# Kernel tuning notes

Measured on AMD Instinct MI355X. Metric: run time of the kernel, lower is better.

## Reference

```python
import jax, jax.numpy as jnp
import numpy as np

EPS = 1e-3  # BatchNorm eps from module

def _bn(x, g, b, m, v):
    # torch BatchNorm1d (eval): (x - mean) / sqrt(var + eps) * weight + bias
    return (x - m) * (g / jnp.sqrt(v + EPS)) + b

def setup_inputs() -> dict:
    key = jax.random.key(0)
    ks = jax.random.split(key, 16)
    N, Cin, Cout, S = 1_000_000, 16, 64, 20_000
    inputs = jax.random.normal(ks[0], (N, Cin), dtype=jnp.float32)
    unq_inv = jax.random.randint(ks[1], (N,), 0, S, dtype=jnp.int32)

    def bn_params(k, c):
        k1, k2, k3, k4 = jax.random.split(k, 4)
        return (1.0 + 0.01 * jax.random.normal(k1, (c,), jnp.float32),
                0.01 * jax.random.normal(k2, (c,), jnp.float32),
                0.01 * jax.random.normal(k3, (c,), jnp.float32),
                jax.random.uniform(k4, (c,), jnp.float32, 0.5, 1.5))

    W1 = 0.1 * jax.random.normal(ks[2], (Cin, Cout), jnp.float32)
    g1, b1, m1, v1 = bn_params(ks[3], Cout)
    W2a = 0.1 * jax.random.normal(ks[4], (Cin, 2 * Cout), jnp.float32)
    g2a, b2a, m2a, v2a = bn_params(ks[5], 2 * Cout)
    W2b = 0.1 * jax.random.normal(ks[6], (2 * Cout, Cout), jnp.float32)
    g2b, b2b, m2b, v2b = bn_params(ks[7], Cout)

    return dict(inputs=inputs, unq_inv=unq_inv, num_segments=S,
                W1=W1, g1=g1, b1=b1, m1=m1, v1=v1,
                W2a=W2a, g2a=g2a, b2a=b2a, m2a=m2a, v2a=v2a,
                W2b=W2b, g2b=b2b * 0 + g2b, b2b=b2b, m2b=m2b, v2b=v2b)

def reference(inputs, unq_inv, num_segments,
              W1, g1, b1, m1, v1,
              W2a, g2a, b2a, m2a, v2a,
              W2b, g2b, b2b, m2b, v2b):
    # branch 1: Linear -> BN -> ReLU
    x = jax.nn.relu(_bn(inputs @ W1, g1, b1, m1, v1))            # [N, C]
    # branch 2: Linear -> BN -> ReLU -> Linear -> BN -> ReLU
    h = jax.nn.relu(_bn(inputs @ W2a, g2a, b2a, m2a, v2a))       # [N, 2C]
    x2 = jax.nn.relu(_bn(h @ W2b, g2b, b2b, m2b, v2b))           # [N, C]

    # segment reductions over group ids
    x_max = jax.ops.segment_max(x, unq_inv, num_segments=num_segments)  # [S, C]
    x_max = jnp.maximum(x_max, 0.0)  # empty segments -> 0 (x >= 0 post-ReLU)
    group_sum = jax.ops.segment_sum(x, unq_inv, num_segments=num_segments)  # [S, C]
    max_pool = jnp.max(x2, axis=0)                                # [C], global pool
    max_pool = jnp.broadcast_to(max_pool[None, :], x_max.shape)   # [S, C]

    feat = jnp.concatenate((group_sum, x_max, max_pool), axis=1)  # [S, 3C]
    # channel shuffle with groups=3
    S_, C3 = feat.shape
    feat = feat.reshape(S_, 3, C3 // 3).transpose(0, 2, 1).reshape(S_, C3)
    return feat
```

## Files before the change

### kernel.cpp

```cpp
#include <hip/hip_runtime.h>

#define EPS 1e-3f

#define OFF_T2B    7168
#define OFF_MPP    7232
#define OFF_CNT    11392
#define OFF_OFFS   31408
#define OFF_CUR    51424
#define OFF_INPS   71424

typedef short short8 __attribute__((ext_vector_type(8)));
typedef float f32x4 __attribute__((ext_vector_type(4)));

union U4 { unsigned u[4]; short8 s8; uint4 u4; };

__device__ inline unsigned short f2bf(float f) {
    unsigned u = __float_as_uint(f);
    return (unsigned short)((u + 0x7FFFu + ((u >> 16) & 1u)) >> 16);
}

__global__ __launch_bounds__(256) void init_k(
    const float* __restrict__ W1,
    const float* __restrict__ g1, const float* __restrict__ b1,
    const float* __restrict__ m1, const float* __restrict__ v1,
    const float* __restrict__ W2a,
    const float* __restrict__ g2a, const float* __restrict__ b2a,
    const float* __restrict__ m2a, const float* __restrict__ v2a,
    const float* __restrict__ W2b,
    const float* __restrict__ g2b, const float* __restrict__ b2b,
    const float* __restrict__ m2b, const float* __restrict__ v2b,
    unsigned short* __restrict__ wsu, float* __restrict__ wsf,
    const int* __restrict__ unq, int* __restrict__ cnt, int N)
{
    const int t = threadIdx.x;
    if (blockIdx.x == 0) {
        for (int i = t; i < 2048; i += 256) {
            int mt = i >> 9, lane = (i >> 3) & 63, j = i & 7;
            int c = lane & 15, g = lane >> 4;
            int k = g * 8 + j, ch = mt * 16 + c;
            float s = g1[ch] * rsqrtf(v1[ch] + EPS);
            float val = (k < 16) ? W1[k * 64 + ch] * s
                      : (k == 16 ? b1[ch] - m1[ch] * s : 0.f);
            wsu[i] = f2bf(val);
        }
        for (int i = t; i < 4096; i += 256) {
            int mt = i >> 9, lane = (i >> 3) & 63, j = i & 7;
            int c = lane & 15, g = lane >> 4;
            int k = g * 8 + j, ch = mt * 16 + c;
            float s = g2a[ch] * rsqrtf(v2a[ch] + EPS);
            float val = (k < 16) ? W2a[k * 128 + ch] * s
                      : (k == 16 ? b2a[ch] - m2a[ch] * s : 0.f);
            wsu[2048 + i] = f2bf(val);
        }
        for (int i = t; i < 8192; i += 256) {
            int f = i >> 9, lane = (i >> 3) & 63, j = i & 7;
            int mt = f >> 2, ks = f & 3;
            int c = lane & 15, g = lane >> 4;
            int k = ks * 32 + g * 8 + j, ch = mt * 16 + c;
            float s = g2b[ch] * rsqrtf(v2b[ch] + EPS);
            wsu[6144 + i] = f2bf(W2b[k * 64 + ch] * s);
        }
        if (t < 64) {
            float s = g2b[t] * rsqrtf(v2b[t] + EPS);
            wsf[OFF_T2B + t] = b2b[t] - m2b[t] * s;
        }
    } else {
        const int i = (blockIdx.x - 1) * 256 + t;
        if (i < N) atomicAdd(&cnt[unq[i]], 1);
    }
}

__global__ __launch_bounds__(1024) void scan_k(
    const int* __restrict__ cnt, int* __restrict__ offs,
    int* __restrict__ cur, int S)
{
    __shared__ int tot[1024];
    const int t = threadIdx.x;
    const int E = (S + 1023) >> 10;
    const int i0 = t * E;
    int run = 0;
    for (int j = 0; j < E; ++j) {
        const int i = i0 + j;
        run += (i < S) ? cnt[i] : 0;
    }
    tot[t] = run;
    __syncthreads();
    for (int d = 1; d < 1024; d <<= 1) {
        int x = (t >= d) ? tot[t - d] : 0;
        __syncthreads();
        tot[t] += x;
        __syncthreads();
    }
    int base = (t == 0) ? 0 : tot[t - 1];
    for (int j = 0; j < E; ++j) {
        const int i = i0 + j;
        if (i < S) {
            offs[i] = base;
            cur[i]  = base;
            base += cnt[i];
        }
    }
    if (t == 1023) offs[S] = tot[1023];
}

__device__ __forceinline__ void b2_tile(
    const U4& bf, bool act, const short8 (&w2a)[8],
    const char* __restrict__ w2bs, char* __restrict__ scr,
    float (&mp)[16], int lane, int c, int g)
{
    const f32x4 zero4 = {0.f, 0.f, 0.f, 0.f};
    __builtin_amdgcn_wave_barrier();
    #pragma unroll
    for (int mt = 0; mt < 8; ++mt) {
        f32x4 hT = __builtin_amdgcn_mfma_f32_16x16x32_bf16(w2a[mt], bf.s8, zero4, 0, 0, 0);
        float h0 = fmaxf(hT[0], 0.f), h1 = fmaxf(hT[1], 0.f);
        float h2 = fmaxf(hT[2], 0.f), h3 = fmaxf(hT[3], 0.f);
        unsigned lo, hi;
        asm("v_cvt_pk_bf16_f32 %0, %1, %2" : "=v"(lo) : "v"(h0), "v"(h1));
        asm("v_cvt_pk_bf16_f32 %0, %1, %2" : "=v"(hi) : "v"(h2), "v"(h3));
        const int gw = 2 * (mt & 1) + (g >> 1);
        *reinterpret_cast<uint2*>(
            &scr[(mt >> 1) * 1024 + (gw * 16 + c) * 16 + (g & 1) * 8])
            = make_uint2(lo, hi);
    }
    __builtin_amdgcn_wave_barrier();
    f32x4 y2t[4];
    #pragma unroll
    for (int mt = 0; mt < 4; ++mt) y2t[mt] = zero4;
    #pragma unroll
    for (int ks = 0; ks < 4; ++ks) {
        short8 hb = *reinterpret_cast<const short8*>(&scr[ks * 1024 + lane * 16]);
        #pragma unroll
        for (int mt = 0; mt < 4; ++mt) {
            short8 a = *reinterpret_cast<const short8*>(
                &w2bs[((mt * 4 + ks) * 64 + lane) * 16]);
            y2t[mt] = __builtin_amdgcn_mfma_f32_16x16x32_bf16(a, hb, y2t[mt], 0, 0, 0);
        }
    }
    #pragma unroll
    for (int mt = 0; mt < 4; ++mt) {
        #pragma unroll
        for (int r = 0; r < 4; ++r)
            mp[mt * 4 + r] = act ? fmaxf(mp[mt * 4 + r], y2t[mt][r]) : mp[mt * 4 + r];
    }
}

__global__ __launch_bounds__(256, 4) void brscat_k(
    const float* __restrict__ inputs,
    const int*   __restrict__ unq,
    int*         __restrict__ cur,
    uint4*       __restrict__ inpS,
    const uint4* __restrict__ wsw,
    const float* __restrict__ wsf,
    float* __restrict__ mpp,
    int N)
{
    __shared__ __align__(16) char w2bs[16384];
    __shared__ __align__(16) char scrs[4][4096];
    __shared__ float mpb[64];

    const int tid  = threadIdx.x;
    const int wv   = tid >> 6;
    const int lane = tid & 63;
    const int c = lane & 15;
    const int g = lane >> 4;

    #pragma unroll
    for (int u = 0; u < 4; ++u)
        reinterpret_cast<uint4*>(w2bs)[u * 256 + tid] = wsw[768 + u * 256 + tid];
    if (tid < 64) mpb[tid] = 0.f;
    __syncthreads();

    short8 w2a[8];
    #pragma unroll
    for (int s = 0; s < 8; ++s) {
        U4 t; t.u4 = wsw[256 + s * 64 + lane]; w2a[s] = t.s8;
    }
    #pragma unroll
    for (int s = 0; s < 8; ++s) asm volatile("" : "+v"(w2a[s]));

    char* scr = scrs[wv];
    float mp[16];
    #pragma unroll
    for (int j = 0; j < 16; ++j) mp[j] = -3.0e38f;

    const long stride = (long)gridDim.x * 256;
    for (long base = (long)blockIdx.x * 256 + (long)wv * 64; base < N; base += stride) {
        const long nrem = (long)N - base;

        const long ip = base + lane;
        int pos = 0;
        if (ip < (long)N) pos = atomicAdd(&cur[unq[ip]], 1);

        #pragma unroll
        for (int ti = 0; ti < 4; ++ti) {
            if ((long)ti * 16 >= nrem) break;
            const bool act = (long)(ti * 16 + c) < nrem;

            U4 bf;
            if (g < 2) {
                const long row = act ? (base + ti * 16 + c) : (long)(N - 1);
                const float4* p = reinterpret_cast<const float4*>(inputs + row * 16 + g * 8);
                float4 q0 = p[0], q1 = p[1];
                asm("v_cvt_pk_bf16_f32 %0, %1, %2" : "=v"(bf.u[0]) : "v"(q0.x), "v"(q0.y));
                asm("v_cvt_pk_bf16_f32 %0, %1, %2" : "=v"(bf.u[1]) : "v"(q0.z), "v"(q0.w));
                asm("v_cvt_pk_bf16_f32 %0, %1, %2" : "=v"(bf.u[2]) : "v"(q1.x), "v"(q1.y));
                asm("v_cvt_pk_bf16_f32 %0, %1, %2" : "=v"(bf.u[3]) : "v"(q1.z), "v"(q1.w));
                if (!act) { bf.u[0] = 0u; bf.u[1] = 0u; bf.u[2] = 0u; bf.u[3] = 0u; }
            } else {
                bf.u[0] = (g == 2 && act) ? 0x00003F80u : 0u;
                bf.u[1] = 0u; bf.u[2] = 0u; bf.u[3] = 0u;
            }

            const int posc = __shfl(pos, ti * 16 + c, 64);
            if (g < 2 && act)
                inpS[(size_t)posc * 2 + g] = bf.u4;

            b2_tile(bf, act, w2a, w2bs, scr, mp, lane, c, g);
        }
    }

    #pragma unroll
    for (int j = 0; j < 16; ++j) {
        float x = mp[j];
        x = fmaxf(x, __shfl_xor(x, 1, 64));
        x = fmaxf(x, __shfl_xor(x, 2, 64));
        x = fmaxf(x, __shfl_xor(x, 4, 64));
        x = fmaxf(x, __shfl_xor(x, 8, 64));
        mp[j] = x;
    }
    if (c == 0) {
        #pragma unroll
        for (int mt = 0; mt < 4; ++mt)
            #pragma unroll
            for (int r = 0; r < 4; ++r) {
                const int ch = mt * 16 + g * 4 + r;
                const float v = fmaxf(mp[mt * 4 + r] + wsf[OFF_T2B + ch], 0.f);
                atomicMax(reinterpret_cast<int*>(&mpb[ch]), __float_as_int(v));
            }
    }
    __syncthreads();
    if (tid < 64)
        atomicMax(reinterpret_cast<int*>(mpp + (blockIdx.x & 63) * 64 + tid),
                  __float_as_int(mpb[tid]));
}

__global__ __launch_bounds__(256, 4) void seg1_k(
    const uint4* __restrict__ inpS,
    const int*   __restrict__ offs,
    const uint4* __restrict__ wsw,
    const float* __restrict__ mpp,
    float* __restrict__ out,
    int S)
{
    __shared__ float scr3[4][192];

    const int tid  = threadIdx.x;
    const int wv   = tid >> 6;
    const int lane = tid & 63;
    const int c = lane & 15;
    const int g = lane >> 4;

    short8 w1[4];
    #pragma unroll
    for (int mt = 0; mt < 4; ++mt) {
        U4 t; t.u4 = wsw[mt * 64 + lane]; w1[mt] = t.s8;
    }
    float mpl = 0.f;
    #pragma unroll
    for (int s = 0; s < 64; ++s)
        mpl = fmaxf(mpl, mpp[s * 64 + lane]);

    float* sr = scr3[wv];
    const f32x4 zero4 = {0.f, 0.f, 0.f, 0.f};

    const int nw = gridDim.x * 4;
    for (int seg = blockIdx.x * 4 + wv; seg < S; seg += nw) {
        const int su    = __builtin_amdgcn_readfirstlane(seg);
        const int start = offs[su];
        const int end   = offs[su + 1];

        f32x4 as[4], am[4];
        #pragma unroll
        for (int mt = 0; mt < 4; ++mt) { as[mt] = zero4; am[mt] = zero4; }

        for (int base = start; base < end; base += 64) {
            const int nrem = end - base;
            #pragma unroll
            for (int ti = 0; ti < 4; ++ti) {
                if (ti * 16 >= nrem) break;
                const bool act = (ti * 16 + c) < nrem;

                U4 bf;
                if (g < 2) {
                    const int row = min(base + ti * 16 + c, end - 1);
                    uint4 q = inpS[(size_t)row * 2 + g];
                    bf.u[0] = act ? q.x : 0u;
                    bf.u[1] = act ? q.y : 0u;
                    bf.u[2] = act ? q.z : 0u;
                    bf.u[3] = act ? q.w : 0u;
                } else {
                    bf.u[0] = (g == 2 && act) ? 0x00003F80u : 0u;
                    bf.u[1] = 0u; bf.u[2] = 0u; bf.u[3] = 0u;
                }
                #pragma unroll
                for (int mt = 0; mt < 4; ++mt) {
                    f32x4 y1t = __builtin_amdgcn_mfma_f32_16x16x32_bf16(w1[mt], bf.s8, zero4, 0, 0, 0);
                    #pragma unroll
                    for (int r = 0; r < 4; ++r) {
                        float v = fmaxf(y1t[r], 0.f);
                        as[mt][r] += v;
                        am[mt][r]  = fmaxf(am[mt][r], v);
                    }
                }
            }
        }

        #pragma unroll
        for (int mt = 0; mt < 4; ++mt) {
            #pragma unroll
            for (int r = 0; r < 4; ++r) {
                float xs = as[mt][r], xm = am[mt][r];
                xs += __shfl_xor(xs, 1, 64);  xm = fmaxf(xm, __shfl_xor(xm, 1, 64));
                xs += __shfl_xor(xs, 2, 64);  xm = fmaxf(xm, __shfl_xor(xm, 2, 64));
                xs += __shfl_xor(xs, 4, 64);  xm = fmaxf(xm, __shfl_xor(xm, 4, 64));
                xs += __shfl_xor(xs, 8, 64);  xm = fmaxf(xm, __shfl_xor(xm, 8, 64));
                as[mt][r] = xs; am[mt][r] = xm;
            }
        }

        if (c == 0) {
            #pragma unroll
            for (int mt = 0; mt < 4; ++mt)
                #pragma unroll
                for (int r = 0; r < 4; ++r) {
                    const int ch = mt * 16 + g * 4 + r;
                    sr[ch * 3 + 0] = as[mt][r];
                    sr[ch * 3 + 1] = am[mt][r];
                }
        }
        sr[lane * 3 + 2] = mpl;
        __builtin_amdgcn_wave_barrier();
        asm volatile("s_waitcnt lgkmcnt(0)" ::: "memory");
        __builtin_amdgcn_sched_barrier(0);

        float* o = out + (size_t)seg * 192;
        #pragma unroll
        for (int p = 0; p < 3; ++p)
            o[p * 64 + lane] = sr[p * 64 + lane];
        __builtin_amdgcn_wave_barrier();
    }
}

extern "C" void kernel_launch(void* const* d_in, const int* in_sizes, int n_in,
                              void* d_out, int out_size, void* d_ws, size_t ws_size,
                              hipStream_t stream)
{
    const float* inputs = (const float*)d_in[0];
    const int*   unq    = (const int*)d_in[1];
    const float* W1  = (const float*)d_in[3];
    const float* g1  = (const float*)d_in[4];
    const float* b1  = (const float*)d_in[5];
    const float* m1  = (const float*)d_in[6];
    const float* v1  = (const float*)d_in[7];
    const float* W2a = (const float*)d_in[8];
    const float* g2a = (const float*)d_in[9];
    const float* b2a = (const float*)d_in[10];
    const float* m2a = (const float*)d_in[11];
    const float* v2a = (const float*)d_in[12];
    const float* W2b = (const float*)d_in[13];
    const float* g2b = (const float*)d_in[14];
    const float* b2b = (const float*)d_in[15];
    const float* m2b = (const float*)d_in[16];
    const float* v2b = (const float*)d_in[17];

    float* wsf = (float*)d_ws;
    float* out = (float*)d_out;
    const int N = in_sizes[0] / 16;
    const int S = out_size / 192;

    float* mpp  = wsf + OFF_MPP;
    int*   cnt  = (int*)(wsf + OFF_CNT);
    int*   offs = (int*)(wsf + OFF_OFFS);
    int*   cur  = (int*)(wsf + OFF_CUR);
    uint4* inpS = (uint4*)(wsf + OFF_INPS);

    hipMemsetAsync(mpp, 0, (size_t)(OFF_CNT + 20016 - OFF_MPP) * sizeof(float), stream);

    init_k<<<1 + (N + 255) / 256, 256, 0, stream>>>(
        W1, g1, b1, m1, v1, W2a, g2a, b2a, m2a, v2a, W2b, g2b, b2b, m2b, v2b,
        (unsigned short*)d_ws, wsf, unq, cnt, N);

    scan_k<<<1, 1024, 0, stream>>>(cnt, offs, cur, S);

    brscat_k<<<1024, 256, 0, stream>>>(inputs, unq, cur, inpS,
                                       (const uint4*)d_ws, wsf, mpp, N);

    seg1_k<<<1024, 256, 0, stream>>>(inpS, offs, (const uint4*)d_ws,
                                     mpp, out, S);
}
```

Baseline: 213.4 us.

## Transpose MFMA operand roles to shrink accumulators and raise occupancy

```diff
diff --git a/kernel.cpp b/kernel.cpp
--- a/kernel.cpp
+++ b/kernel.cpp
@@ -35,9 +35,9 @@
     const int t = threadIdx.x;
     if (blockIdx.x == 0) {
         for (int i = t; i < 2048; i += 256) {
-            int mt = i >> 9, lane = (i >> 3) & 63, j = i & 7;
+            int tt = i >> 9, lane = (i >> 3) & 63, j = i & 7;
             int c = lane & 15, g = lane >> 4;
-            int k = g * 8 + j, ch = mt * 16 + c;
+            int k = g * 8 + j, ch = tt * 16 + c;
             float s = g1[ch] * rsqrtf(v1[ch] + EPS);
             float val = (k < 16) ? W1[k * 64 + ch] * s
                       : (k == 16 ? b1[ch] - m1[ch] * s : 0.f);
@@ -54,9 +54,9 @@
         }
         for (int i = t; i < 8192; i += 256) {
             int f = i >> 9, lane = (i >> 3) & 63, j = i & 7;
-            int mt = f >> 2, ks = f & 3;
+            int ks = f >> 2, tt = f & 3;
             int c = lane & 15, g = lane >> 4;
-            int k = ks * 32 + g * 8 + j, ch = mt * 16 + c;
+            int k = ks * 32 + g * 8 + j, ch = tt * 16 + c;
             float s = g2b[ch] * rsqrtf(v2b[ch] + EPS);
             wsu[6144 + i] = f2bf(W2b[k * 64 + ch] * s);
         }
@@ -104,48 +104,56 @@
 }
 
 __device__ __forceinline__ void b2_tile(
-    const U4& bf, bool act, const short8 (&w2a)[8],
+    const U4& bf, const short8 (&w2a)[8],
     const char* __restrict__ w2bs, char* __restrict__ scr,
-    float (&mp)[16], int lane, int c, int g)
+    float (&mp)[4], int lane, int c, int g, bool act, int pt_lim)
 {
     const f32x4 zero4 = {0.f, 0.f, 0.f, 0.f};
-    __builtin_amdgcn_wave_barrier();
-    #pragma unroll
-    for (int mt = 0; mt < 8; ++mt) {
-        f32x4 hT = __builtin_amdgcn_mfma_f32_16x16x32_bf16(w2a[mt], bf.s8, zero4, 0, 0, 0);
-        float h0 = fmaxf(hT[0], 0.f), h1 = fmaxf(hT[1], 0.f);
-        float h2 = fmaxf(hT[2], 0.f), h3 = fmaxf(hT[3], 0.f);
-        unsigned lo, hi;
-        asm("v_cvt_pk_bf16_f32 %0, %1, %2" : "=v"(lo) : "v"(h0), "v"(h1));
-        asm("v_cvt_pk_bf16_f32 %0, %1, %2" : "=v"(hi) : "v"(h2), "v"(h3));
-        const int gw = 2 * (mt & 1) + (g >> 1);
-        *reinterpret_cast<uint2*>(
-            &scr[(mt >> 1) * 1024 + (gw * 16 + c) * 16 + (g & 1) * 8])
-            = make_uint2(lo, hi);
-    }
-    __builtin_amdgcn_wave_barrier();
     f32x4 y2t[4];
     #pragma unroll
-    for (int mt = 0; mt < 4; ++mt) y2t[mt] = zero4;
-    #pragma unroll
-    for (int ks = 0; ks < 4; ++ks) {
-        short8 hb = *reinterpret_cast<const short8*>(&scr[ks * 1024 + lane * 16]);
-        #pragma unroll
-        for (int mt = 0; mt < 4; ++mt) {
-            short8 a = *reinterpret_cast<const short8*>(
-                &w2bs[((mt * 4 + ks) * 64 + lane) * 16]);
-            y2t[mt] = __builtin_amdgcn_mfma_f32_16x16x32_bf16(a, hb, y2t[mt], 0, 0, 0);
-        }
-    }
-    #pragma unroll
-    for (int mt = 0; mt < 4; ++mt) {
-        #pragma unroll
-        for (int r = 0; r < 4; ++r)
-            mp[mt * 4 + r] = act ? fmaxf(mp[mt * 4 + r], y2t[mt][r]) : mp[mt * 4 + r];
-    }
-}
-
-__global__ __launch_bounds__(256, 4) void brscat_k(
+    for (int tt = 0; tt < 4; ++tt) y2t[tt] = zero4;
+
+    #pragma unroll
+    for (int half = 0; half < 2; ++half) {
+        __builtin_amdgcn_wave_barrier();
+        #pragma unroll
+        for (int m = 0; m < 4; ++m) {
+            const int mt = half * 4 + m;
+            f32x4 hT = __builtin_amdgcn_mfma_f32_16x16x32_bf16(w2a[mt], bf.s8, zero4, 0, 0, 0);
+            float h0 = fmaxf(hT[0], 0.f), h1 = fmaxf(hT[1], 0.f);
+            float h2 = fmaxf(hT[2], 0.f), h3 = fmaxf(hT[3], 0.f);
+            unsigned lo, hi;
+            asm("v_cvt_pk_bf16_f32 %0, %1, %2" : "=v"(lo) : "v"(h0), "v"(h1));
+            asm("v_cvt_pk_bf16_f32 %0, %1, %2" : "=v"(hi) : "v"(h2), "v"(h3));
+            const int gw = 2 * (mt & 1) + (g >> 1);
+            *reinterpret_cast<uint2*>(
+                &scr[((mt >> 1) & 1) * 1024 + (gw * 16 + c) * 16 + (g & 1) * 8])
+                = make_uint2(lo, hi);
+        }
+        __builtin_amdgcn_wave_barrier();
+        #pragma unroll
+        for (int ksl = 0; ksl < 2; ++ksl) {
+            short8 hb = *reinterpret_cast<const short8*>(&scr[ksl * 1024 + lane * 16]);
+            const int ks = half * 2 + ksl;
+            #pragma unroll
+            for (int tt = 0; tt < 4; ++tt) {
+                short8 b = *reinterpret_cast<const short8*>(
+                    &w2bs[((ks * 4 + tt) * 64 + lane) * 16]);
+                y2t[tt] = __builtin_amdgcn_mfma_f32_16x16x32_bf16(hb, b, y2t[tt], 0, 0, 0);
+            }
+        }
+    }
+    if (act) {
+        #pragma unroll
+        for (int tt = 0; tt < 4; ++tt)
+            #pragma unroll
+            for (int r = 0; r < 4; ++r)
+                if (g * 4 + r < pt_lim)
+                    mp[tt] = fmaxf(mp[tt], y2t[tt][r]);
+    }
+}
+
+__global__ __launch_bounds__(256, 5) void brscat_k(
     const float* __restrict__ inputs,
     const int*   __restrict__ unq,
     int*         __restrict__ cur,
@@ -156,7 +164,7 @@
     int N)
 {
     __shared__ __align__(16) char w2bs[16384];
-    __shared__ __align__(16) char scrs[4][4096];
+    __shared__ __align__(16) char scrs[4][2048];
     __shared__ float mpb[64];
 
     const int tid  = threadIdx.x;
@@ -180,64 +188,81 @@
     for (int s = 0; s < 8; ++s) asm volatile("" : "+v"(w2a[s]));
 
     char* scr = scrs[wv];
-    float mp[16];
-    #pragma unroll
-    for (int j = 0; j < 16; ++j) mp[j] = -3.0e38f;
-
+    float mp[4];
+    #pragma unroll
+    for (int j = 0; j < 4; ++j) mp[j] = -3.0e38f;
+
+    const unsigned loff = (unsigned)(c * 64 + g * 32);
     const long stride = (long)gridDim.x * 256;
     for (long base = (long)blockIdx.x * 256 + (long)wv * 64; base < N; base += stride) {
         const long nrem = (long)N - base;
 
-        const long ip = base + lane;
-        int pos = 0;
-        if (ip < (long)N) pos = atomicAdd(&cur[unq[ip]], 1);
-
-        #pragma unroll
-        for (int ti = 0; ti < 4; ++ti) {
-            if ((long)ti * 16 >= nrem) break;
-            const bool act = (long)(ti * 16 + c) < nrem;
-
-            U4 bf;
-            if (g < 2) {
-                const long row = act ? (base + ti * 16 + c) : (long)(N - 1);
-                const float4* p = reinterpret_cast<const float4*>(inputs + row * 16 + g * 8);
-                float4 q0 = p[0], q1 = p[1];
-                asm("v_cvt_pk_bf16_f32 %0, %1, %2" : "=v"(bf.u[0]) : "v"(q0.x), "v"(q0.y));
-                asm("v_cvt_pk_bf16_f32 %0, %1, %2" : "=v"(bf.u[1]) : "v"(q0.z), "v"(q0.w));
-                asm("v_cvt_pk_bf16_f32 %0, %1, %2" : "=v"(bf.u[2]) : "v"(q1.x), "v"(q1.y));
-                asm("v_cvt_pk_bf16_f32 %0, %1, %2" : "=v"(bf.u[3]) : "v"(q1.z), "v"(q1.w));
-                if (!act) { bf.u[0] = 0u; bf.u[1] = 0u; bf.u[2] = 0u; bf.u[3] = 0u; }
-            } else {
-                bf.u[0] = (g == 2 && act) ? 0x00003F80u : 0u;
-                bf.u[1] = 0u; bf.u[2] = 0u; bf.u[3] = 0u;
+        if (nrem >= 64) {
+            const int pos = atomicAdd(&cur[unq[base + lane]], 1);
+            const char* bp = reinterpret_cast<const char*>(inputs + base * 16);
+            #pragma unroll
+            for (int ti = 0; ti < 4; ++ti) {
+                U4 bf;
+                if (g < 2) {
+                    float4 q0 = *reinterpret_cast<const float4*>(bp + loff + ti * 1024);
+                    float4 q1 = *reinterpret_cast<const float4*>(bp + loff + ti * 1024 + 16);
+                    asm("v_cvt_pk_bf16_f32 %0, %1, %2" : "=v"(bf.u[0]) : "v"(q0.x), "v"(q0.y));
+                    asm("v_cvt_pk_bf16_f32 %0, %1, %2" : "=v"(bf.u[1]) : "v"(q0.z), "v"(q0.w));
+                    asm("v_cvt_pk_bf16_f32 %0, %1, %2" : "=v"(bf.u[2]) : "v"(q1.x), "v"(q1.y));
+                    asm("v_cvt_pk_bf16_f32 %0, %1, %2" : "=v"(bf.u[3]) : "v"(q1.z), "v"(q1.w));
+                } else {
+                    bf.u[0] = (g == 2) ? 0x00003F80u : 0u;
+                    bf.u[1] = 0u; bf.u[2] = 0u; bf.u[3] = 0u;
+                }
+                const int posc = __shfl(pos, ti * 16 + c, 64);
+                if (g < 2)
+                    inpS[(size_t)posc * 2 + g] = bf.u4;
+                b2_tile(bf, w2a, w2bs, scr, mp, lane, c, g, true, 16);
             }
-
-            const int posc = __shfl(pos, ti * 16 + c, 64);
-            if (g < 2 && act)
-                inpS[(size_t)posc * 2 + g] = bf.u4;
-
-            b2_tile(bf, act, w2a, w2bs, scr, mp, lane, c, g);
-        }
-    }
-
-    #pragma unroll
-    for (int j = 0; j < 16; ++j) {
-        float x = mp[j];
-        x = fmaxf(x, __shfl_xor(x, 1, 64));
-        x = fmaxf(x, __shfl_xor(x, 2, 64));
-        x = fmaxf(x, __shfl_xor(x, 4, 64));
-        x = fmaxf(x, __shfl_xor(x, 8, 64));
-        mp[j] = x;
-    }
-    if (c == 0) {
-        #pragma unroll
-        for (int mt = 0; mt < 4; ++mt)
-            #pragma unroll
-            for (int r = 0; r < 4; ++r) {
-                const int ch = mt * 16 + g * 4 + r;
-                const float v = fmaxf(mp[mt * 4 + r] + wsf[OFF_T2B + ch], 0.f);
-                atomicMax(reinterpret_cast<int*>(&mpb[ch]), __float_as_int(v));
+        } else {
+            int pos = 0;
+            if (lane < nrem) pos = atomicAdd(&cur[unq[base + lane]], 1);
+            #pragma unroll
+            for (int ti = 0; ti < 4; ++ti) {
+                if ((long)ti * 16 >= nrem) break;
+                const bool act = (long)(ti * 16 + c) < nrem;
+                U4 bf;
+                if (g < 2) {
+                    const long row = act ? (base + ti * 16 + c) : base;
+                    const float4* p = reinterpret_cast<const float4*>(inputs + row * 16 + g * 8);
+                    float4 q0 = p[0], q1 = p[1];
+                    asm("v_cvt_pk_bf16_f32 %0, %1, %2" : "=v"(bf.u[0]) : "v"(q0.x), "v"(q0.y));
+                    asm("v_cvt_pk_bf16_f32 %0, %1, %2" : "=v"(bf.u[1]) : "v"(q0.z), "v"(q0.w));
+                    asm("v_cvt_pk_bf16_f32 %0, %1, %2" : "=v"(bf.u[2]) : "v"(q1.x), "v"(q1.y));
+                    asm("v_cvt_pk_bf16_f32 %0, %1, %2" : "=v"(bf.u[3]) : "v"(q1.z), "v"(q1.w));
+                    if (!act) { bf.u[0] = 0u; bf.u[1] = 0u; bf.u[2] = 0u; bf.u[3] = 0u; }
+                } else {
+                    bf.u[0] = (g == 2 && act) ? 0x00003F80u : 0u;
+                    bf.u[1] = 0u; bf.u[2] = 0u; bf.u[3] = 0u;
+                }
+                const int posc = __shfl(pos, ti * 16 + c, 64);
+                if (g < 2 && act)
+                    inpS[(size_t)posc * 2 + g] = bf.u4;
+                const int pl = (int)min((long)16, nrem - (long)ti * 16);
+                b2_tile(bf, w2a, w2bs, scr, mp, lane, c, g, true, pl);
             }
+        }
+    }
+
+    #pragma unroll
+    for (int tt = 0; tt < 4; ++tt) {
+        float x = mp[tt];
+        x = fmaxf(x, __shfl_xor(x, 16, 64));
+        x = fmaxf(x, __shfl_xor(x, 32, 64));
+        mp[tt] = x;
+    }
+    if (g == 0) {
+        #pragma unroll
+        for (int tt = 0; tt < 4; ++tt) {
+            const int ch = tt * 16 + c;
+            const float v = fmaxf(mp[tt] + wsf[OFF_T2B + ch], 0.f);
+            atomicMax(reinterpret_cast<int*>(&mpb[ch]), __float_as_int(v));
+        }
     }
     __syncthreads();
     if (tid < 64)
@@ -245,7 +270,7 @@
                   __float_as_int(mpb[tid]));
 }
 
-__global__ __launch_bounds__(256, 4) void seg1_k(
+__global__ __launch_bounds__(256, 6) void seg1_k(
     const uint4* __restrict__ inpS,
     const int*   __restrict__ offs,
     const uint4* __restrict__ wsw,
@@ -263,8 +288,8 @@
 
     short8 w1[4];
     #pragma unroll
-    for (int mt = 0; mt < 4; ++mt) {
-        U4 t; t.u4 = wsw[mt * 64 + lane]; w1[mt] = t.s8;
+    for (int tt = 0; tt < 4; ++tt) {
+        U4 t; t.u4 = wsw[tt * 64 + lane]; w1[tt] = t.s8;
     }
     float mpl = 0.f;
     #pragma unroll
@@ -280,9 +305,9 @@
         const int start = offs[su];
         const int end   = offs[su + 1];
 
-        f32x4 as[4], am[4];
-        #pragma unroll
-        for (int mt = 0; mt < 4; ++mt) { as[mt] = zero4; am[mt] = zero4; }
+        float as[4], am[4];
+        #pragma unroll
+        for (int tt = 0; tt < 4; ++tt) { as[tt] = 0.f; am[tt] = 0.f; }
 
         for (int base = start; base < end; base += 64) {
             const int nrem = end - base;
@@ -293,7 +318,7 @@
 
                 U4 bf;
                 if (g < 2) {
-                    const int row = min(base + ti * 16 + c, end - 1);
+                    const int row = act ? (base + ti * 16 + c) : start;
                     uint4 q = inpS[(size_t)row * 2 + g];
                     bf.u[0] = act ? q.x : 0u;
                     bf.u[1] = act ? q.y : 0u;
@@ -304,40 +329,33 @@
                     bf.u[1] = 0u; bf.u[2] = 0u; bf.u[3] = 0u;
                 }
                 #pragma unroll
-                for (int mt = 0; mt < 4; ++mt) {
-                    f32x4 y1t = __builtin_amdgcn_mfma_f32_16x16x32_bf16(w1[mt], bf.s8, zero4, 0, 0, 0);
+                for (int tt = 0; tt < 4; ++tt) {
+                    f32x4 y1t = __builtin_amdgcn_mfma_f32_16x16x32_bf16(bf.s8, w1[tt], zero4, 0, 0, 0);
                     #pragma unroll
                     for (int r = 0; r < 4; ++r) {
                         float v = fmaxf(y1t[r], 0.f);
-                        as[mt][r] += v;
-                        am[mt][r]  = fmaxf(am[mt][r], v);
+                        as[tt] += v;
+                        am[tt]  = fmaxf(am[tt], v);
                     }
                 }
             }
         }
 
         #pragma unroll
-        for (int mt = 0; mt < 4; ++mt) {
-            #pragma unroll
-            for (int r = 0; r < 4; ++r) {
-                float xs = as[mt][r], xm = am[mt][r];
-                xs += __shfl_xor(xs, 1, 64);  xm = fmaxf(xm, __shfl_xor(xm, 1, 64));
-                xs += __shfl_xor(xs, 2, 64);  xm = fmaxf(xm, __shfl_xor(xm, 2, 64));
-                xs += __shfl_xor(xs, 4, 64);  xm = fmaxf(xm, __shfl_xor(xm, 4, 64));
-                xs += __shfl_xor(xs, 8, 64);  xm = fmaxf(xm, __shfl_xor(xm, 8, 64));
-                as[mt][r] = xs; am[mt][r] = xm;
+        for (int tt = 0; tt < 4; ++tt) {
+            float xs = as[tt], xm = am[tt];
+            xs += __shfl_xor(xs, 16, 64);  xm = fmaxf(xm, __shfl_xor(xm, 16, 64));
+            xs += __shfl_xor(xs, 32, 64);  xm = fmaxf(xm, __shfl_xor(xm, 32, 64));
+            as[tt] = xs; am[tt] = xm;
+        }
+
+        if (g == 0) {
+            #pragma unroll
+            for (int tt = 0; tt < 4; ++tt) {
+                const int ch = tt * 16 + c;
+                sr[ch * 3 + 0] = as[tt];
+                sr[ch * 3 + 1] = am[tt];
             }
-        }
-
-        if (c == 0) {
-            #pragma unroll
-            for (int mt = 0; mt < 4; ++mt)
-                #pragma unroll
-                for (int r = 0; r < 4; ++r) {
-                    const int ch = mt * 16 + g * 4 + r;
-                    sr[ch * 3 + 0] = as[mt][r];
-                    sr[ch * 3 + 1] = am[mt][r];
-                }
         }
         sr[lane * 3 + 2] = mpl;
         __builtin_amdgcn_wave_barrier();
@@ -393,9 +411,9 @@
 
     scan_k<<<1, 1024, 0, stream>>>(cnt, offs, cur, S);
 
-    brscat_k<<<1024, 256, 0, stream>>>(inputs, unq, cur, inpS,
+    brscat_k<<<2048, 256, 0, stream>>>(inputs, unq, cur, inpS,
                                        (const uint4*)d_ws, wsf, mpp, N);
 
-    seg1_k<<<1024, 256, 0, stream>>>(inpS, offs, (const uint4*)d_ws,
+    seg1_k<<<2048, 256, 0, stream>>>(inpS, offs, (const uint4*)d_ws,
                                      mpp, out, S);
 }
```

New measurement: 213.9 us. No clear change (+0.3%).
